# Kernel optimization log

Hardware: AMD Instinct MI355X
Metric: run time of the kernel (lower is better)

## Reference

```python
import jax, jax.numpy as jnp
import numpy as np

N_BASE = 4          # len('NACGT'[1:])
STATE_LEN = 5
S = N_BASE ** STATE_LEN   # 1024 states
NZ = N_BASE + 1           # 5 transitions per state
T_STEPS = 800
BATCH = 32


def _build_idx():
    # idx[i] = [i, 0*256 + i//4, 1*256 + i//4, 2*256 + i//4, 3*256 + i//4]
    i = np.arange(S)
    trans = np.stack([j * (S // N_BASE) + i // N_BASE for j in range(N_BASE)], axis=1)
    idx = np.concatenate([i[:, None], trans], axis=1).astype(np.int64)      # (S, NZ)
    # transposed transition structure (stable sort: duplicates grouped deterministically)
    idx_T = np.argsort(idx.ravel(), kind='stable').reshape(S, NZ)
    idx_T_div = idx_T // NZ
    return jnp.asarray(idx), jnp.asarray(idx_T), jnp.asarray(idx_T_div)


def _scan(Ms, idx, v0):
    """Log-semiring recurrence: alpha[t+1] = logsumexp(Ms[t] + alpha[t][:, idx], -1).
    Ms: (T, N, S, NZ); idx: (S, NZ); v0: (N, S). Returns (T+1, N, S)."""
    def step(alpha, M):
        nxt = jax.scipy.special.logsumexp(M + alpha[:, idx], axis=-1)  # (N, S)
        return nxt, nxt
    _, alphas = jax.lax.scan(step, v0, Ms)
    return jnp.concatenate([v0[None], alphas], axis=0)


def setup_inputs() -> dict:
    key = jax.random.key(0)
    scores = jax.random.normal(key, (T_STEPS, BATCH, S * NZ), dtype=jnp.float32)
    return {"scores": scores}


def reference(scores):
    idx, idx_T, idx_T_div = _build_idx()
    T, N, _ = scores.shape
    Ms = scores.reshape(T, N, S, NZ)
    v0 = jnp.zeros((N, S), scores.dtype)   # semiring Log.one == 0.0
    # forward scores
    fwd = _scan(Ms, idx, v0)                                   # (T+1, N, S)
    # backward scores: gather transposed transitions, run scan in reverse time
    Ms_T = scores[:, :, idx_T]                                 # (T, N, S, NZ)
    bwd = jnp.flip(_scan(jnp.flip(Ms_T, 0), idx_T_div, v0), 0)  # (T+1, N, S)
    posts = jax.nn.softmax(fwd + bwd, axis=-1)                 # (T+1, N, S)
    return (jnp.swapaxes(scores, 0, 1),
            jnp.swapaxes(bwd, 0, 1),
            jnp.swapaxes(posts, 0, 1))
```

## Files before the change

kernel.cpp:

```cpp
#include <hip/hip_runtime.h>
#include <stdint.h>

#define T_STEPS 800
#define NBATCH  32
#define SST     1024
#define ROW     5120
#define RING    5

#define SCAN_BLOCKS 64
#define COPY_BLOCKS 1536
#define GRID (SCAN_BLOCKS + COPY_BLOCKS)

__device__ __forceinline__ float lse5(float v0, float v1, float v2, float v3, float v4) {
  float m = fmaxf(fmaxf(fmaxf(v0, v1), fmaxf(v2, v3)), v4);
  float s = __expf(v0 - m) + __expf(v1 - m) + __expf(v2 - m) +
            __expf(v3 - m) + __expf(v4 - m);
  return m + __logf(s);
}

#define WAITVM(N) do { \
  asm volatile("s_waitcnt vmcnt(" #N ")" ::: "memory"); \
  __builtin_amdgcn_sched_barrier(0); } while (0)

__device__ __forceinline__ void barrier_lgkm() {
  asm volatile("s_waitcnt lgkmcnt(0)" ::: "memory");
  __builtin_amdgcn_s_barrier();
  asm volatile("" ::: "memory");
}

__device__ __forceinline__ void stage16(const float* g, float* l) {
  __builtin_amdgcn_global_load_lds(
      (const __attribute__((address_space(1))) uint32_t*)g,
      (__attribute__((address_space(3))) uint32_t*)l, 16, 0, 0);
}

__device__ __forceinline__ void stage_row(const float* __restrict__ rowg,
                                          float* __restrict__ ldsrow,
                                          int w, int lane) {
  const float* src = rowg + 1280 * w + 4 * lane;
  float* dst = ldsrow + 1280 * w;
#pragma unroll
  for (int k = 0; k < 5; ++k) stage16(src + 256 * k, dst + 256 * k);
}

template <int DIR, int PHASE>
__device__ __forceinline__ void step_one(int s, int buf, int u, int w, int lane,
                                         const float* __restrict__ base,
                                         float* __restrict__ outn,
                                         float (*ring)[ROW], float (*abuf)[SST],
                                         float (&a)[4]) {
  if constexpr (PHASE == 0)      WAITVM(21);
  else if constexpr (PHASE == 1) { if constexpr (DIR) WAITVM(36); else WAITVM(24); }
  else                           WAITVM(0);

  if constexpr (DIR) barrier_lgkm();

  const int cur = s & 1;
  const int nxt = cur ^ 1;
  const float* rb = ring[buf];

  float4 q[5];
  const float4* rv = (const float4*)(rb + 20 * u);
#pragma unroll
  for (int m = 0; m < 5; ++m) q[m] = rv[m];
  float fv[20];
#pragma unroll
  for (int m = 0; m < 5; ++m) {
    fv[4 * m + 0] = q[m].x; fv[4 * m + 1] = q[m].y;
    fv[4 * m + 2] = q[m].z; fv[4 * m + 3] = q[m].w;
  }
  float sv[4];
  if constexpr (DIR) {
#pragma unroll
    for (int j = 0; j < 4; ++j) sv[j] = rb[5 * u + 1280 * j];
  }

  float4 pv;
  if constexpr (!DIR) {
    pv.x = abuf[cur][u];
    pv.y = abuf[cur][u + 256];
    pv.z = abuf[cur][u + 512];
    pv.w = abuf[cur][u + 768];
  } else {
    pv = *(const float4*)&abuf[cur][4 * u];
  }

  float na[4];
#pragma unroll
  for (int j = 0; j < 4; ++j) {
    float w0, w1, w2, w3, w4;
    if constexpr (!DIR) {
      w0 = fv[5 * j + 0] + a[j];
      w1 = fv[5 * j + 1] + pv.x;
      w2 = fv[5 * j + 2] + pv.y;
      w3 = fv[5 * j + 3] + pv.z;
      w4 = fv[5 * j + 4] + pv.w;
    } else {
      w0 = sv[j]          + a[j];
      w1 = fv[1 + j + 0]  + pv.x;
      w2 = fv[1 + j + 5]  + pv.y;
      w3 = fv[1 + j + 10] + pv.z;
      w4 = fv[1 + j + 15] + pv.w;
    }
    na[j] = lse5(w0, w1, w2, w3, w4);
    a[j] = na[j];
  }

  if constexpr (!DIR) {
    const float4 o = {na[0], na[1], na[2], na[3]};
    ((float4*)(outn + (size_t)(s + 1) * SST))[u] = o;
    *(float4*)&abuf[nxt][4 * u] = o;
  } else {
    const int t = T_STEPS - 1 - s;
#pragma unroll
    for (int j = 0; j < 4; ++j) {
      outn[(size_t)t * SST + u + 256 * j] = na[j];
      abuf[nxt][u + 256 * j] = na[j];
    }
  }

  barrier_lgkm();

  if constexpr (PHASE != 2) {
    const int tn = DIR ? (T_STEPS - 1 - (s + RING)) : (s + RING);
    stage_row(base + (size_t)tn * (NBATCH * ROW), ring[buf], w, lane);
  }
}

template <int DIR>
__device__ void scan_run(const float* __restrict__ scores, float* __restrict__ out,
                         int n, float (*ring)[ROW], float (*abuf)[SST]) {
  const int u = threadIdx.x;
  const int w = u >> 6, lane = u & 63;
  const float* base = scores + (size_t)n * ROW;
  float* outn = out + (size_t)n * (T_STEPS + 1) * SST;
  float a[4] = {0.f, 0.f, 0.f, 0.f};

#pragma unroll
  for (int i = 0; i < RING; ++i) {
    const int t = DIR ? (T_STEPS - 1 - i) : i;
    stage_row(base + (size_t)t * (NBATCH * ROW), ring[i], w, lane);
  }
  {
    const float4 z = {0.f, 0.f, 0.f, 0.f};
    *(float4*)&abuf[0][4 * u] = z;
    const size_t t0 = DIR ? (size_t)T_STEPS : 0;
    ((float4*)(outn + t0 * SST))[u] = z;
  }
  barrier_lgkm();

#pragma unroll
  for (int i = 0; i < RING; ++i)
    step_one<DIR, 0>(i, i, u, w, lane, base, outn, ring, abuf, a);

  for (int p = RING; p < T_STEPS - RING; p += RING) {
#pragma unroll
    for (int i = 0; i < RING; ++i)
      step_one<DIR, 1>(p + i, i, u, w, lane, base, outn, ring, abuf, a);
  }

#pragma unroll
  for (int i = 0; i < RING; ++i)
    step_one<DIR, 2>(T_STEPS - RING + i, i, u, w, lane, base, outn, ring, abuf, a);
}

__global__ __launch_bounds__(256) void mega(const float* __restrict__ scores,
                                            float* __restrict__ out0,
                                            float* __restrict__ bwdo,
                                            float* __restrict__ fposts) {
  __shared__ float ring[RING][ROW];
  __shared__ float abuf[2][SST];
  const int b = blockIdx.x;
  if (b < SCAN_BLOCKS) {
    if (b < NBATCH) scan_run<0>(scores, fposts, b, ring, abuf);
    else            scan_run<1>(scores, bwdo,   b - NBATCH, ring, abuf);
  } else {
    const int tb = b - SCAN_BLOCKS;
    for (int r = tb; r < NBATCH * T_STEPS; r += COPY_BLOCKS) {
      const int t = r / NBATCH, n = r % NBATCH;
      const float4* src = (const float4*)(scores + (size_t)r * ROW);
      float4* dst = (float4*)(out0 + ((size_t)n * T_STEPS + t) * ROW);
#pragma unroll
      for (int i = 0; i < 5; ++i)
        dst[threadIdx.x + 256 * i] = src[threadIdx.x + 256 * i];
    }
  }
}

__global__ __launch_bounds__(256) void posts_kernel(float* __restrict__ fp,
                                                    const float* __restrict__ bp) {
  const int lane = threadIdx.x & 63;
  const int wid  = threadIdx.x >> 6;
  const size_t row = (size_t)blockIdx.x * 4 + wid;
  float* f = fp + row * SST;
  const float* b = bp + row * SST;

  float x[16];
#pragma unroll
  for (int k = 0; k < 4; ++k) {
    const float4 fv = ((const float4*)f)[lane + 64 * k];
    const float4 bv = ((const float4*)b)[lane + 64 * k];
    x[4 * k + 0] = fv.x + bv.x;
    x[4 * k + 1] = fv.y + bv.y;
    x[4 * k + 2] = fv.z + bv.z;
    x[4 * k + 3] = fv.w + bv.w;
  }
  float m = x[0];
#pragma unroll
  for (int j = 1; j < 16; ++j) m = fmaxf(m, x[j]);
#pragma unroll
  for (int off = 32; off >= 1; off >>= 1) m = fmaxf(m, __shfl_xor(m, off));
  float ssum = 0.0f;
#pragma unroll
  for (int j = 0; j < 16; ++j) { x[j] = __expf(x[j] - m); ssum += x[j]; }
#pragma unroll
  for (int off = 32; off >= 1; off >>= 1) ssum += __shfl_xor(ssum, off);
  const float inv = 1.0f / ssum;
#pragma unroll
  for (int k = 0; k < 4; ++k) {
    float4 o;
    o.x = x[4 * k + 0] * inv;
    o.y = x[4 * k + 1] * inv;
    o.z = x[4 * k + 2] * inv;
    o.w = x[4 * k + 3] * inv;
    ((float4*)f)[lane + 64 * k] = o;
  }
}

extern "C" void kernel_launch(void* const* d_in, const int* in_sizes, int n_in,
                              void* d_out, int out_size, void* d_ws, size_t ws_size,
                              hipStream_t stream) {
  (void)in_sizes; (void)n_in; (void)d_ws; (void)ws_size; (void)out_size;
  const float* scores = (const float*)d_in[0];
  float* out = (float*)d_out;
  float* out0   = out;
  float* bwdo   = out + (size_t)NBATCH * T_STEPS * ROW;
  float* fposts = bwdo + (size_t)NBATCH * (T_STEPS + 1) * SST;

  mega<<<GRID, 256, 0, stream>>>(scores, out0, bwdo, fposts);
  posts_kernel<<<(NBATCH * (T_STEPS + 1)) / 4, 256, 0, stream>>>(fposts, bwdo);
}
```

Baseline: 694.1 us.

## Fuse scores transpose-copy into scan blocks from LDS ring buffer

Drops the separate 1536 copy blocks that re-read scores from global memory. The forward and backward scan blocks now write the transposed scores output straight from the rows already staged in LDS, with forward taking even chunks and backward taking odd chunks. This removes a second full read of scores and stops the copy blocks competing with the scans for bandwidth. In exchange, extra global stores go onto the serial scan critical path, and the vmcnt wait thresholds were raised to account for them.

After: 703.5 us. About the same (+1.3%).

```diff
diff --git a/kernel.cpp b/kernel.cpp
--- a/kernel.cpp
+++ b/kernel.cpp
@@ -8,8 +8,6 @@
 #define RING    5
 
 #define SCAN_BLOCKS 64
-#define COPY_BLOCKS 1536
-#define GRID (SCAN_BLOCKS + COPY_BLOCKS)
 
 __device__ __forceinline__ float lse5(float v0, float v1, float v2, float v3, float v4) {
   float m = fmaxf(fmaxf(fmaxf(v0, v1), fmaxf(v2, v3)), v4);
@@ -45,18 +43,20 @@
 
 template <int DIR, int PHASE>
 __device__ __forceinline__ void step_one(int s, int buf, int u, int w, int lane,
+                                         float* __restrict__ outn,
+                                         float* __restrict__ o0n,
                                          const float* __restrict__ base,
-                                         float* __restrict__ outn,
                                          float (*ring)[ROW], float (*abuf)[SST],
                                          float (&a)[4]) {
   if constexpr (PHASE == 0)      WAITVM(21);
-  else if constexpr (PHASE == 1) { if constexpr (DIR) WAITVM(36); else WAITVM(24); }
+  else if constexpr (PHASE == 1) { if constexpr (DIR) WAITVM(44); else WAITVM(36); }
   else                           WAITVM(0);
 
   if constexpr (DIR) barrier_lgkm();
 
   const int cur = s & 1;
   const int nxt = cur ^ 1;
+  const int t = DIR ? (T_STEPS - 1 - s) : s;
   const float* rb = ring[buf];
 
   float4 q[5];
@@ -106,12 +106,25 @@
     a[j] = na[j];
   }
 
+  {
+    float* o0 = o0n + (size_t)t * ROW + 1280 * w + 4 * lane;
+    const float* qb = rb + 1280 * w + 4 * lane;
+    if constexpr (!DIR) {
+#pragma unroll
+      for (int c = 0; c < 5; c += 2)
+        *(float4*)(o0 + 256 * c) = *(const float4*)(qb + 256 * c);
+    } else {
+#pragma unroll
+      for (int c = 1; c < 5; c += 2)
+        *(float4*)(o0 + 256 * c) = *(const float4*)(qb + 256 * c);
+    }
+  }
+
   if constexpr (!DIR) {
     const float4 o = {na[0], na[1], na[2], na[3]};
     ((float4*)(outn + (size_t)(s + 1) * SST))[u] = o;
     *(float4*)&abuf[nxt][4 * u] = o;
   } else {
-    const int t = T_STEPS - 1 - s;
 #pragma unroll
     for (int j = 0; j < 4; ++j) {
       outn[(size_t)t * SST + u + 256 * j] = na[j];
@@ -129,11 +142,13 @@
 
 template <int DIR>
 __device__ void scan_run(const float* __restrict__ scores, float* __restrict__ out,
-                         int n, float (*ring)[ROW], float (*abuf)[SST]) {
+                         float* __restrict__ out0, int n,
+                         float (*ring)[ROW], float (*abuf)[SST]) {
   const int u = threadIdx.x;
   const int w = u >> 6, lane = u & 63;
   const float* base = scores + (size_t)n * ROW;
   float* outn = out + (size_t)n * (T_STEPS + 1) * SST;
+  float* o0n  = out0 + (size_t)n * T_STEPS * ROW;
   float a[4] = {0.f, 0.f, 0.f, 0.f};
 
 #pragma unroll
@@ -151,17 +166,17 @@
 
 #pragma unroll
   for (int i = 0; i < RING; ++i)
-    step_one<DIR, 0>(i, i, u, w, lane, base, outn, ring, abuf, a);
+    step_one<DIR, 0>(i, i, u, w, lane, outn, o0n, base, ring, abuf, a);
 
   for (int p = RING; p < T_STEPS - RING; p += RING) {
 #pragma unroll
     for (int i = 0; i < RING; ++i)
-      step_one<DIR, 1>(p + i, i, u, w, lane, base, outn, ring, abuf, a);
+      step_one<DIR, 1>(p + i, i, u, w, lane, outn, o0n, base, ring, abuf, a);
   }
 
 #pragma unroll
   for (int i = 0; i < RING; ++i)
-    step_one<DIR, 2>(T_STEPS - RING + i, i, u, w, lane, base, outn, ring, abuf, a);
+    step_one<DIR, 2>(T_STEPS - RING + i, i, u, w, lane, outn, o0n, base, ring, abuf, a);
 }
 
 __global__ __launch_bounds__(256) void mega(const float* __restrict__ scores,
@@ -171,20 +186,8 @@
   __shared__ float ring[RING][ROW];
   __shared__ float abuf[2][SST];
   const int b = blockIdx.x;
-  if (b < SCAN_BLOCKS) {
-    if (b < NBATCH) scan_run<0>(scores, fposts, b, ring, abuf);
-    else            scan_run<1>(scores, bwdo,   b - NBATCH, ring, abuf);
-  } else {
-    const int tb = b - SCAN_BLOCKS;
-    for (int r = tb; r < NBATCH * T_STEPS; r += COPY_BLOCKS) {
-      const int t = r / NBATCH, n = r % NBATCH;
-      const float4* src = (const float4*)(scores + (size_t)r * ROW);
-      float4* dst = (float4*)(out0 + ((size_t)n * T_STEPS + t) * ROW);
-#pragma unroll
-      for (int i = 0; i < 5; ++i)
-        dst[threadIdx.x + 256 * i] = src[threadIdx.x + 256 * i];
-    }
-  }
+  if (b < NBATCH) scan_run<0>(scores, fposts, out0, b, ring, abuf);
+  else            scan_run<1>(scores, bwdo,   out0, b - NBATCH, ring, abuf);
 }
 
 __global__ __launch_bounds__(256) void posts_kernel(float* __restrict__ fp,
@@ -237,6 +240,6 @@
   float* bwdo   = out + (size_t)NBATCH * T_STEPS * ROW;
   float* fposts = bwdo + (size_t)NBATCH * (T_STEPS + 1) * SST;
 
-  mega<<<GRID, 256, 0, stream>>>(scores, out0, bwdo, fposts);
+  mega<<<SCAN_BLOCKS, 256, 0, stream>>>(scores, out0, bwdo, fposts);
   posts_kernel<<<(NBATCH * (T_STEPS + 1)) / 4, 256, 0, stream>>>(fposts, bwdo);
 }
```
